# Optimization experiments

Hardware: AMD Instinct MI355X
Metric: run time of the kernel (lower is better)

## Reference

```python
import math
import jax, jax.numpy as jnp
import numpy as np

B, C, NX, NY = 8, 16, 512, 512
N = 16384
N_RES, NH, S = 90, 5, 0.5


def _normal(x, mu, s):
    # exp(-0.5*((x-mu)/s)^2) / (sqrt(s^2) * sqrt(2*pi))  -- matches torch helper
    return jnp.exp(-0.5 * ((x - mu) / s) ** 2) / (jnp.sqrt(s * s) * math.sqrt(2.0 * math.pi))


def setup_inputs() -> dict:
    key = jax.random.key(0)
    k1, k2 = jax.random.split(key)
    x = jax.random.normal(k1, (B, C, NX, NY), dtype=jnp.float32)
    coords = jax.random.uniform(k2, (B, N, 2), dtype=jnp.float32)
    nh_m = (NH - 1) / 2 + 0.5
    pixel_offset_normal = jnp.linspace(nh_m, -nh_m, N_RES, dtype=jnp.float32)
    pixel_offset_indices = jnp.linspace(-(NH - 1) // 2, (NH - 1) // 2, NH, dtype=jnp.float32)
    s = jnp.float32(S)
    return {"x": x, "coords": coords, "s": s,
            "pixel_offset_normal": pixel_offset_normal,
            "pixel_offset_indices": pixel_offset_indices}


def reference(x, coords, s, pixel_offset_normal, pixel_offset_indices):
    b, n, _ = coords.shape
    _, c, nx, ny = x.shape
    nh = pixel_offset_indices.shape[0]

    # continuous positions in pixel space
    px = coords[:, :, 1] * (nx - 1)   # [b,n]
    py = coords[:, :, 0] * (ny - 1)
    rpx, rpy = jnp.round(px), jnp.round(py)

    # gaussian weights integrated over sub-pixel resolution (n_res samples -> nh bins)
    # NOTE: torch code clamps both axes with x.shape[-2] (=nx); replicated faithfully.
    pxo = jnp.clip(rpx[..., None] - pixel_offset_normal, 0.0, nx)   # [b,n,n_res]
    pyo = jnp.clip(rpy[..., None] - pixel_offset_normal, 0.0, nx)
    wx = _normal(pxo, px[..., None], s).reshape(b, n, nh, -1).sum(-1)  # [b,n,nh]
    wy = _normal(pyo, py[..., None], s).reshape(b, n, nh, -1).sum(-1)
    w2d = wx[..., :, None] * wy[..., None, :]                          # [b,n,nh,nh]
    w2d = w2d / w2d.reshape(b, n, -1).sum(-1)[..., None, None]

    # integer neighborhood indices (both axes clamped with nx-1, as in torch code)
    ix = jnp.clip(jnp.round(rpx[..., None] - pixel_offset_indices), 0, nx - 1).astype(jnp.int32)  # [b,n,nh]
    iy = jnp.clip(jnp.round(rpy[..., None] - pixel_offset_indices), 0, nx - 1).astype(jnp.int32)

    # per-batch gather of nh x nh neighborhoods (equivalent to torch's BxB gather + diagonal)
    flat = (ix[..., :, None] * ny + iy[..., None, :]).reshape(b, n * nh * nh)  # [b, n*nh*nh]
    xf = x.reshape(b, c, nx * ny)
    g = jax.vmap(lambda xi, idx: xi[:, idx])(xf, flat)       # [b,c,n*nh*nh]
    g = g.reshape(b, c, n, nh, nh)

    out = (g * w2d[:, None]).reshape(b, c, n, nh * nh).sum(-1)  # [b,c,n]
    return out
```

## Files before the change

### kernel.cpp

```cpp
#include <hip/hip_runtime.h>

#define BV    8
#define CV    16
#define NXV   512
#define NYV   512
#define NV    16384
#define NRES  90
#define NHV   5
#define TPB   256

#define NPTS  (BV * NV)
#define TSH   3
#define TDIM  (NXV >> TSH)
#define NBUCKB (TDIM * TDIM)
#define NBUCK  (BV * NBUCKB)
#define SCANT 1024
#define SPT   (NBUCK / SCANT)

#if __has_builtin(__builtin_amdgcn_exp2f)
#define EXP2 __builtin_amdgcn_exp2f
#else
#define EXP2 exp2f
#endif

__global__ void zero_counts_kernel(int* __restrict__ counts) {
    int i = blockIdx.x * blockDim.x + threadIdx.x;
    if (i < NBUCK) counts[i] = 0;
}

__global__ __launch_bounds__(TPB) void bucket_count_kernel(
    const float* __restrict__ coords, int* __restrict__ counts,
    int* __restrict__ keys)
{
    const int i = blockIdx.x * TPB + threadIdx.x;
    const float2 cd = *(const float2*)(coords + (size_t)i * 2);
    const float rpx = rintf(cd.y * (float)(NXV - 1));
    const float rpy = rintf(cd.x * (float)(NYV - 1));
    const unsigned tx = ((unsigned)(int)rpx) >> TSH;
    const unsigned ty = ((unsigned)(int)rpy) >> TSH;
    unsigned m = 0;
    #pragma unroll
    for (int k = 0; k < 6; ++k)
        m |= (((tx >> k) & 1u) << (2 * k)) | (((ty >> k) & 1u) << (2 * k + 1));
    const int key = (i >> 14) * NBUCKB + (int)m;
    keys[i] = key;
    atomicAdd(&counts[key], 1);
}

__global__ __launch_bounds__(SCANT) void scan_kernel(
    const int* __restrict__ counts, int* __restrict__ cursors)
{
    __shared__ int sm[SCANT];
    const int tid  = threadIdx.x;
    const int base = tid * SPT;

    int v[SPT];
    int run = 0;
    #pragma unroll
    for (int k = 0; k < SPT; ++k) {
        v[k] = run;
        run += counts[base + k];
    }
    sm[tid] = run;
    __syncthreads();
    #pragma unroll
    for (int off = 1; off < SCANT; off <<= 1) {
        int t = sm[tid];
        if (tid >= off) t += sm[tid - off];
        __syncthreads();
        sm[tid] = t;
        __syncthreads();
    }
    const int tbase = sm[tid] - run;
    #pragma unroll
    for (int k = 0; k < SPT; ++k)
        cursors[base + k] = tbase + v[k];
}

__global__ __launch_bounds__(TPB) void scatter_kernel(
    const int* __restrict__ keys, int* __restrict__ cursors,
    int* __restrict__ order)
{
    const int i = blockIdx.x * TPB + threadIdx.x;
    const int pos = atomicAdd(&cursors[keys[i]], 1);
    order[pos] = i;
}

__global__ __launch_bounds__(TPB) void weights_kernel(
    const float* __restrict__ coords,
    const float* __restrict__ s_ptr,
    const float* __restrict__ offn,
    const float* __restrict__ offi,
    const int*   __restrict__ order,
    float4* __restrict__ w8a, float4* __restrict__ w8b,
    float4* __restrict__ wx4, float* __restrict__ wx1,
    int4*   __restrict__ off4, int* __restrict__ off1,
    int*    __restrict__ idx)
{
    const int p = blockIdx.x * TPB + threadIdx.x;
    const int i = order[p];

    const float2 cd = *(const float2*)(coords + (size_t)i * 2);
    const float px  = cd.y * (float)(NXV - 1);
    const float py  = cd.x * (float)(NYV - 1);
    const float rpx = rintf(px);
    const float rpy = rintf(py);

    const float s = s_ptr[0];
    const float k = -0.72134752044448169f / (s * s);

    float wx[NHV], wy[NHV];
    float sx = 0.f, sy = 0.f;
    #pragma unroll
    for (int h = 0; h < NHV; ++h) {
        float ax = 0.f, ay = 0.f;
        #pragma unroll 6
        for (int t = 0; t < NRES / NHV; ++t) {
            const float off = offn[h * (NRES / NHV) + t];
            const float vx = fminf(fmaxf(rpx - off, 0.f), (float)NXV);
            const float vy = fminf(fmaxf(rpy - off, 0.f), (float)NXV);
            const float dx = vx - px;
            const float dy = vy - py;
            ax += EXP2(k * dx * dx);
            ay += EXP2(k * dy * dy);
        }
        wx[h] = ax; wy[h] = ay;
        sx += ax;  sy += ay;
    }
    const float inv = 1.0f / (sx * sy);

    int ix[NHV], iy[NHV];
    #pragma unroll
    for (int h = 0; h < NHV; ++h) {
        const float fo = offi[h];
        ix[h] = (int)fminf(fmaxf(rintf(rpx - fo), 0.f), (float)(NXV - 1));
        iy[h] = (int)fminf(fmaxf(rintf(rpy - fo), 0.f), (float)(NXV - 1));
    }

    const int a = min(iy[NHV - 1] & ~3, NYV - 8);

    float w8[8];
    #pragma unroll
    for (int kk = 0; kk < 8; ++kk) {
        float w = 0.f;
        #pragma unroll
        for (int j = 0; j < NHV; ++j)
            w += (iy[j] - a == kk) ? wy[j] * inv : 0.f;
        w8[kk] = w;
    }

    w8a[p] = make_float4(w8[0], w8[1], w8[2], w8[3]);
    w8b[p] = make_float4(w8[4], w8[5], w8[6], w8[7]);
    wx4[p] = make_float4(wx[0], wx[1], wx[2], wx[3]);
    wx1[p] = wx[4];
    off4[p] = make_int4((ix[0] * NYV + a) * 4, (ix[1] * NYV + a) * 4,
                        (ix[2] * NYV + a) * 4, (ix[3] * NYV + a) * 4);
    off1[p] = (ix[4] * NYV + a) * 4;
    idx[p]  = i;
}

__global__ __launch_bounds__(TPB) void gather_kernel(
    const float* __restrict__ x,
    const float4* __restrict__ w8a, const float4* __restrict__ w8b,
    const float4* __restrict__ wx4, const float* __restrict__ wx1,
    const int4*   __restrict__ off4, const int* __restrict__ off1,
    const int*    __restrict__ idx,
    float* __restrict__ out)
{
    const int nwg = NPTS / TPB;
    const int bid = blockIdx.x;
    const int swz = (bid & 7) * (nwg / 8) + (bid >> 3);
    const int p   = swz * TPB + threadIdx.x;
    const int c   = blockIdx.y;

    const float4 wa = w8a[p];
    const float4 wb = w8b[p];
    const float4 wr = wx4[p];
    const float  we = wx1[p];
    const int4   o4 = off4[p];
    const int    oe = off1[p];
    const int    i  = idx[p];
    const int    b  = i >> 14;
    const int    n  = i & (NV - 1);

    const char* base = (const char*)x + ((size_t)(b * CV + c) << 20);

    float acc = 0.f;
#define ROW(OFF, WROW) {                                                    \
        const float4* rp = (const float4*)(base + (size_t)(unsigned)(OFF)); \
        const float4 va = rp[0];                                            \
        const float4 vb = rp[1];                                            \
        const float rs = va.x * wa.x + va.y * wa.y + va.z * wa.z +          \
                         va.w * wa.w + vb.x * wb.x + vb.y * wb.y +          \
                         vb.z * wb.z + vb.w * wb.w;                         \
        acc = fmaf(WROW, rs, acc); }

    ROW(o4.x, wr.x)
    ROW(o4.y, wr.y)
    ROW(o4.z, wr.z)
    ROW(o4.w, wr.w)
    ROW(oe,   we)
#undef ROW

    out[(((size_t)(b * CV + c)) << 14) + n] = acc;
}

extern "C" void kernel_launch(void* const* d_in, const int* in_sizes, int n_in,
                              void* d_out, int out_size, void* d_ws, size_t ws_size,
                              hipStream_t stream) {
    const float* x      = (const float*)d_in[0];
    const float* coords = (const float*)d_in[1];
    const float* s_ptr  = (const float*)d_in[2];
    const float* offn   = (const float*)d_in[3];
    const float* offi   = (const float*)d_in[4];
    float* out = (float*)d_out;

    char* w = (char*)d_ws;
    float4* w8a  = (float4*)w;  w += (size_t)NPTS * 16;
    float4* w8b  = (float4*)w;  w += (size_t)NPTS * 16;
    float4* wx4  = (float4*)w;  w += (size_t)NPTS * 16;
    int4*   off4 = (int4*)w;    w += (size_t)NPTS * 16;
    float*  wx1  = (float*)w;   w += (size_t)NPTS * 4;
    int*    off1 = (int*)w;     w += (size_t)NPTS * 4;
    int*    idx  = (int*)w;     w += (size_t)NPTS * 4;
    int*    counts  = (int*)w;  w += (size_t)NBUCK * 4;
    int*    cursors = (int*)w;  w += (size_t)NBUCK * 4;
    int*    keys    = (int*)w;  w += (size_t)NPTS * 4;
    int*    order   = (int*)w;

    zero_counts_kernel<<<dim3(NBUCK / TPB), dim3(TPB), 0, stream>>>(counts);
    bucket_count_kernel<<<dim3(NPTS / TPB), dim3(TPB), 0, stream>>>(coords, counts, keys);
    scan_kernel<<<dim3(1), dim3(SCANT), 0, stream>>>(counts, cursors);
    scatter_kernel<<<dim3(NPTS / TPB), dim3(TPB), 0, stream>>>(keys, cursors, order);
    weights_kernel<<<dim3(NPTS / TPB), dim3(TPB), 0, stream>>>(
        coords, s_ptr, offn, offi, order, w8a, w8b, wx4, wx1, off4, off1, idx);

    dim3 grid(NPTS / TPB, CV, 1);
    gather_kernel<<<grid, dim3(TPB), 0, stream>>>(
        x, w8a, w8b, wx4, wx1, off4, off1, idx, out);
}
```

Measured before the change: 264.0 us.

## Fuse scatter into weights kernel and process four channels per gather thread

New measurement: 287.9 us. +9.0%, slower.

```diff
diff --git a/kernel.cpp b/kernel.cpp
--- a/kernel.cpp
+++ b/kernel.cpp
@@ -8,6 +8,7 @@
 #define NRES  90
 #define NHV   5
 #define TPB   256
+#define CPERT 4
 
 #define NPTS  (BV * NV)
 #define TSH   3
@@ -28,23 +29,24 @@
     if (i < NBUCK) counts[i] = 0;
 }
 
+__device__ __forceinline__ int bucket_key(float rpx, float rpy, int i) {
+    const unsigned tx = ((unsigned)(int)rpx) >> TSH;
+    const unsigned ty = ((unsigned)(int)rpy) >> TSH;
+    unsigned m = 0;
+    #pragma unroll
+    for (int k = 0; k < 6; ++k)
+        m |= (((tx >> k) & 1u) << (2 * k)) | (((ty >> k) & 1u) << (2 * k + 1));
+    return (i >> 14) * NBUCKB + (int)m;
+}
+
 __global__ __launch_bounds__(TPB) void bucket_count_kernel(
-    const float* __restrict__ coords, int* __restrict__ counts,
-    int* __restrict__ keys)
+    const float* __restrict__ coords, int* __restrict__ counts)
 {
     const int i = blockIdx.x * TPB + threadIdx.x;
     const float2 cd = *(const float2*)(coords + (size_t)i * 2);
     const float rpx = rintf(cd.y * (float)(NXV - 1));
     const float rpy = rintf(cd.x * (float)(NYV - 1));
-    const unsigned tx = ((unsigned)(int)rpx) >> TSH;
-    const unsigned ty = ((unsigned)(int)rpy) >> TSH;
-    unsigned m = 0;
-    #pragma unroll
-    for (int k = 0; k < 6; ++k)
-        m |= (((tx >> k) & 1u) << (2 * k)) | (((ty >> k) & 1u) << (2 * k + 1));
-    const int key = (i >> 14) * NBUCKB + (int)m;
-    keys[i] = key;
-    atomicAdd(&counts[key], 1);
+    atomicAdd(&counts[bucket_key(rpx, rpy, i)], 1);
 }
 
 __global__ __launch_bounds__(SCANT) void scan_kernel(
@@ -77,34 +79,25 @@
         cursors[base + k] = tbase + v[k];
 }
 
-__global__ __launch_bounds__(TPB) void scatter_kernel(
-    const int* __restrict__ keys, int* __restrict__ cursors,
-    int* __restrict__ order)
-{
-    const int i = blockIdx.x * TPB + threadIdx.x;
-    const int pos = atomicAdd(&cursors[keys[i]], 1);
-    order[pos] = i;
-}
-
-__global__ __launch_bounds__(TPB) void weights_kernel(
+__global__ __launch_bounds__(TPB) void scatter_weights_kernel(
     const float* __restrict__ coords,
     const float* __restrict__ s_ptr,
     const float* __restrict__ offn,
     const float* __restrict__ offi,
-    const int*   __restrict__ order,
+    int* __restrict__ cursors,
     float4* __restrict__ w8a, float4* __restrict__ w8b,
-    float4* __restrict__ wx4, float* __restrict__ wx1,
-    int4*   __restrict__ off4, int* __restrict__ off1,
-    int*    __restrict__ idx)
-{
-    const int p = blockIdx.x * TPB + threadIdx.x;
-    const int i = order[p];
+    float4* __restrict__ wx4, int4* __restrict__ off4,
+    float4* __restrict__ misc)
+{
+    const int i = blockIdx.x * TPB + threadIdx.x;
 
     const float2 cd = *(const float2*)(coords + (size_t)i * 2);
     const float px  = cd.y * (float)(NXV - 1);
     const float py  = cd.x * (float)(NYV - 1);
     const float rpx = rintf(px);
     const float rpy = rintf(py);
+
+    const int pos = atomicAdd(&cursors[bucket_key(rpx, rpy, i)], 1);
 
     const float s = s_ptr[0];
     const float k = -0.72134752044448169f / (s * s);
@@ -149,60 +142,65 @@
         w8[kk] = w;
     }
 
-    w8a[p] = make_float4(w8[0], w8[1], w8[2], w8[3]);
-    w8b[p] = make_float4(w8[4], w8[5], w8[6], w8[7]);
-    wx4[p] = make_float4(wx[0], wx[1], wx[2], wx[3]);
-    wx1[p] = wx[4];
-    off4[p] = make_int4((ix[0] * NYV + a) * 4, (ix[1] * NYV + a) * 4,
-                        (ix[2] * NYV + a) * 4, (ix[3] * NYV + a) * 4);
-    off1[p] = (ix[4] * NYV + a) * 4;
-    idx[p]  = i;
-}
-
-__global__ __launch_bounds__(TPB) void gather_kernel(
+    w8a[pos] = make_float4(w8[0], w8[1], w8[2], w8[3]);
+    w8b[pos] = make_float4(w8[4], w8[5], w8[6], w8[7]);
+    wx4[pos] = make_float4(wx[0], wx[1], wx[2], wx[3]);
+    off4[pos] = make_int4((ix[0] * NYV + a) * 4, (ix[1] * NYV + a) * 4,
+                          (ix[2] * NYV + a) * 4, (ix[3] * NYV + a) * 4);
+    misc[pos] = make_float4(wx[4], __int_as_float((ix[4] * NYV + a) * 4),
+                            __int_as_float(i), 0.f);
+}
+
+__global__ __launch_bounds__(TPB, 4) void gather_kernel(
     const float* __restrict__ x,
     const float4* __restrict__ w8a, const float4* __restrict__ w8b,
-    const float4* __restrict__ wx4, const float* __restrict__ wx1,
-    const int4*   __restrict__ off4, const int* __restrict__ off1,
-    const int*    __restrict__ idx,
+    const float4* __restrict__ wx4, const int4* __restrict__ off4,
+    const float4* __restrict__ misc,
     float* __restrict__ out)
 {
     const int nwg = NPTS / TPB;
     const int bid = blockIdx.x;
     const int swz = (bid & 7) * (nwg / 8) + (bid >> 3);
     const int p   = swz * TPB + threadIdx.x;
-    const int c   = blockIdx.y;
+    const int c0  = blockIdx.y * CPERT;
 
     const float4 wa = w8a[p];
     const float4 wb = w8b[p];
     const float4 wr = wx4[p];
-    const float  we = wx1[p];
     const int4   o4 = off4[p];
-    const int    oe = off1[p];
-    const int    i  = idx[p];
+    const float4 ms = misc[p];
+    const float  we = ms.x;
+    const int    oe = __float_as_int(ms.y);
+    const int    i  = __float_as_int(ms.z);
     const int    b  = i >> 14;
     const int    n  = i & (NV - 1);
 
-    const char* base = (const char*)x + ((size_t)(b * CV + c) << 20);
-
-    float acc = 0.f;
-#define ROW(OFF, WROW) {                                                    \
-        const float4* rp = (const float4*)(base + (size_t)(unsigned)(OFF)); \
-        const float4 va = rp[0];                                            \
-        const float4 vb = rp[1];                                            \
-        const float rs = va.x * wa.x + va.y * wa.y + va.z * wa.z +          \
-                         va.w * wa.w + vb.x * wb.x + vb.y * wb.y +          \
-                         vb.z * wb.z + vb.w * wb.w;                         \
-        acc = fmaf(WROW, rs, acc); }
-
-    ROW(o4.x, wr.x)
-    ROW(o4.y, wr.y)
-    ROW(o4.z, wr.z)
-    ROW(o4.w, wr.w)
-    ROW(oe,   we)
-#undef ROW
-
-    out[(((size_t)(b * CV + c)) << 14) + n] = acc;
+    const int   ro[NHV] = {o4.x, o4.y, o4.z, o4.w, oe};
+    const float rw[NHV] = {wr.x, wr.y, wr.z, wr.w, we};
+
+    const char* base = (const char*)x + ((size_t)(b * CV + c0) << 20);
+    float acc[CPERT];
+    #pragma unroll
+    for (int q = 0; q < CPERT; ++q) acc[q] = 0.f;
+
+    #pragma unroll
+    for (int q = 0; q < CPERT; ++q) {
+        const char* bq = base + ((size_t)q << 20);
+        #pragma unroll
+        for (int r = 0; r < NHV; ++r) {
+            const float4* rp = (const float4*)(bq + (size_t)(unsigned)ro[r]);
+            const float4 va = rp[0];
+            const float4 vb = rp[1];
+            const float rs = va.x * wa.x + va.y * wa.y + va.z * wa.z +
+                             va.w * wa.w + vb.x * wb.x + vb.y * wb.y +
+                             vb.z * wb.z + vb.w * wb.w;
+            acc[q] = fmaf(rw[r], rs, acc[q]);
+        }
+    }
+
+    #pragma unroll
+    for (int q = 0; q < CPERT; ++q)
+        out[(((size_t)(b * CV + c0 + q)) << 14) + n] = acc[q];
 }
 
 extern "C" void kernel_launch(void* const* d_in, const int* in_sizes, int n_in,
@@ -220,22 +218,17 @@
     float4* w8b  = (float4*)w;  w += (size_t)NPTS * 16;
     float4* wx4  = (float4*)w;  w += (size_t)NPTS * 16;
     int4*   off4 = (int4*)w;    w += (size_t)NPTS * 16;
-    float*  wx1  = (float*)w;   w += (size_t)NPTS * 4;
-    int*    off1 = (int*)w;     w += (size_t)NPTS * 4;
-    int*    idx  = (int*)w;     w += (size_t)NPTS * 4;
+    float4* misc = (float4*)w;  w += (size_t)NPTS * 16;
     int*    counts  = (int*)w;  w += (size_t)NBUCK * 4;
-    int*    cursors = (int*)w;  w += (size_t)NBUCK * 4;
-    int*    keys    = (int*)w;  w += (size_t)NPTS * 4;
-    int*    order   = (int*)w;
+    int*    cursors = (int*)w;
 
     zero_counts_kernel<<<dim3(NBUCK / TPB), dim3(TPB), 0, stream>>>(counts);
-    bucket_count_kernel<<<dim3(NPTS / TPB), dim3(TPB), 0, stream>>>(coords, counts, keys);
+    bucket_count_kernel<<<dim3(NPTS / TPB), dim3(TPB), 0, stream>>>(coords, counts);
     scan_kernel<<<dim3(1), dim3(SCANT), 0, stream>>>(counts, cursors);
-    scatter_kernel<<<dim3(NPTS / TPB), dim3(TPB), 0, stream>>>(keys, cursors, order);
-    weights_kernel<<<dim3(NPTS / TPB), dim3(TPB), 0, stream>>>(
-        coords, s_ptr, offn, offi, order, w8a, w8b, wx4, wx1, off4, off1, idx);
-
-    dim3 grid(NPTS / TPB, CV, 1);
+    scatter_weights_kernel<<<dim3(NPTS / TPB), dim3(TPB), 0, stream>>>(
+        coords, s_ptr, offn, offi, cursors, w8a, w8b, wx4, off4, misc);
+
+    dim3 grid(NPTS / TPB, CV / CPERT, 1);
     gather_kernel<<<grid, dim3(TPB), 0, stream>>>(
-        x, w8a, w8b, wx4, wx1, off4, off1, idx, out);
-}
+        x, w8a, w8b, wx4, off4, misc, out);
+}
```
